# Optimization experiments

Measured on AMD Instinct MI355X. Metric: run time of the kernel, lower is better.

The kernel has to match this reference:

```python
import jax, jax.numpy as jnp
import numpy as np

B, T, C = 4, 2048, 1024
H, DK, DV = 16, 64, 64


def setup_inputs() -> dict:
    key = jax.random.key(0)
    ks = jax.random.split(key, 12)
    s = 1.0 / np.sqrt(C)
    inp = {
        "Q": jax.random.normal(ks[0], (B, T, C), jnp.float32),
        "K": jax.random.normal(ks[1], (B, T, C), jnp.float32),
        "V": jax.random.normal(ks[2], (B, T, C), jnp.float32),
        # causal mask: True (==1) means masked out
        "mask": jnp.broadcast_to(jnp.triu(jnp.ones((T, T), bool), k=1), (B, 1, T, T)),
        "Wq": jax.random.uniform(ks[3], (C, H * DK), jnp.float32, -s, s),
        "bq": jax.random.uniform(ks[4], (H * DK,), jnp.float32, -s, s),
        "Wk": jax.random.uniform(ks[5], (C, H * DK), jnp.float32, -s, s),
        "bk": jax.random.uniform(ks[6], (H * DK,), jnp.float32, -s, s),
        "Wv": jax.random.uniform(ks[7], (C, H * DV), jnp.float32, -s, s),
        "bv": jax.random.uniform(ks[8], (H * DV,), jnp.float32, -s, s),
        "Wo": jax.random.uniform(ks[9], (H * DV, C), jnp.float32, -s, s),
        "bo": jax.random.uniform(ks[10], (C,), jnp.float32, -s, s),
    }
    return inp


def _split(x, d):
    b, t, _ = x.shape
    return x.reshape(b, t, H, d).transpose(0, 2, 1, 3)  # (B,H,T,d)


def reference(Q, K, V, mask, Wq, bq, Wk, bk, Wv, bv, Wo, bo):
    Qh = _split(Q @ Wq + bq, DK)
    Kh = _split(K @ Wk + bk, DK)
    Vh = _split(V @ Wv + bv, DV)
    scores = jnp.einsum('bhqd,bhkd->bhqk', Qh, Kh) / jnp.sqrt(jnp.float32(DK))
    scores = jnp.where(mask, -jnp.inf, scores)
    attn = jax.nn.softmax(scores, axis=-1)
    out = jnp.einsum('bhqk,bhkd->bhqd', attn, Vh)
    out = out.transpose(0, 2, 1, 3).reshape(B, T, H * DV)
    return out @ Wo + bo
```

## Files before the change

kernel.cpp:

```cpp
#include <hip/hip_runtime.h>
#include <stdint.h>

#define BATCH 4
#define SEQ   2048
#define CH    1024
#define NH    16
#define HD    64

#define QSCALE 0.18033688011112042f

#define GM 8192
#define GN 1024
#define GK 1024

typedef __attribute__((ext_vector_type(8))) short bf16x8;
typedef __attribute__((ext_vector_type(4))) short bf16x4;
typedef __attribute__((ext_vector_type(4))) float f32x4;

__device__ inline unsigned short f2bf(float f) {
    unsigned u = __float_as_uint(f);
    u += 0x7fff + ((u >> 16) & 1);
    return (unsigned short)(u >> 16);
}

__device__ inline float fast_exp2(float x) {
    float r;
    asm("v_exp_f32 %0, %1" : "=v"(r) : "v"(x));
    return r;
}

__device__ inline unsigned cvt_pk_bf16(float lo, float hi) {
    unsigned r;
    asm("v_cvt_pk_bf16_f32 %0, %1, %2" : "=v"(r) : "v"(lo), "v"(hi));
    return r;
}

#if __has_builtin(__builtin_amdgcn_mfma_f32_16x16x16bf16_1k)
__device__ inline void mfma16(f32x4& c, bf16x4 a, bf16x4 b) {
    c = __builtin_amdgcn_mfma_f32_16x16x16bf16_1k(a, b, c, 0, 0, 0);
}
#else
__device__ inline void mfma16(f32x4& c, bf16x4 a, bf16x4 b) {
    asm volatile("s_nop 2\n\tv_mfma_f32_16x16x16_bf16 %0, %1, %2, %0"
                 : "+v"(c) : "v"(a), "v"(b));
}
#endif

__device__ inline void gld_lds16(const void* g, void* l) {
    __builtin_amdgcn_global_load_lds((const __attribute__((address_space(1))) void*)g,
                                     (__attribute__((address_space(3))) void*)l,
                                     16, 0, 0);
}

__global__ __launch_bounds__(256) void prep_k(
    const float* __restrict__ Wq, const float* __restrict__ Wk,
    const float* __restrict__ Wv, const float* __restrict__ Wo,
    unsigned short* __restrict__ WqT, unsigned short* __restrict__ WkT,
    unsigned short* __restrict__ WvT, unsigned short* __restrict__ WoT)
{
    __shared__ float tile[32][33];
    const int j     = blockIdx.x >> 10;
    const int local = blockIdx.x & 1023;
    const float* W = (j == 0) ? Wq : (j == 1) ? Wk : (j == 2) ? Wv : Wo;
    unsigned short* Wt = (j == 0) ? WqT : (j == 1) ? WkT : (j == 2) ? WvT : WoT;
    const int bx = (local & 31) * 32;
    const int by = (local >> 5) * 32;
    const int tx = threadIdx.x & 31;
    const int ty = threadIdx.x >> 5;
#pragma unroll
    for (int i = 0; i < 32; i += 8)
        tile[ty + i][tx] = W[(size_t)(by + ty + i) * CH + bx + tx];
    __syncthreads();
#pragma unroll
    for (int i = 0; i < 32; i += 8)
        Wt[(size_t)(bx + ty + i) * CH + by + tx] = f2bf(tile[tx][ty + i]);
}

__global__ __launch_bounds__(256, 4)
void qkv_gemm(const float* __restrict__ Qf, const float* __restrict__ Kf,
              const float* __restrict__ Vf,
              const unsigned short* __restrict__ WqT, const unsigned short* __restrict__ WkT,
              const unsigned short* __restrict__ WvT,
              const float* __restrict__ bq, const float* __restrict__ bk,
              const float* __restrict__ bv,
              unsigned short* __restrict__ Qhb, unsigned short* __restrict__ Khb,
              unsigned short* __restrict__ Vtb)
{
    __shared__ float          As32[128 * 32];
    __shared__ unsigned short Bs[128 * 32];
    const int job = blockIdx.y;
    const float* A32          = (job == 0) ? Qf  : (job == 1) ? Kf  : Vf;
    const unsigned short* Bt  = (job == 0) ? WqT : (job == 1) ? WkT : WvT;
    const float* bias         = (job == 0) ? bq  : (job == 1) ? bk  : bv;
    unsigned short* outp      = (job == 0) ? Qhb : (job == 1) ? Khb : Vtb;
    const float oscale        = (job == 0) ? QSCALE : 1.0f;

    const int tid  = threadIdx.x;
    const int lane = tid & 63;
    const int w    = tid >> 6;
    const int nbn  = GN >> 7;
    const int nbm  = GM >> 7;
    const int xcd  = blockIdx.x & 7;
    const int idx  = blockIdx.x >> 3;
    const int mb   = xcd * (nbm >> 3) + idx / nbn;
    const int nb   = idx % nbn;
    const int m0   = mb << 7;
    const int n0   = nb << 7;
    const int wrow = (w >> 1) << 6;
    const int wcol = (w & 1) << 6;
    const int lr   = lane & 15;
    const int lg   = lane >> 4;

    f32x4 acc[4][4] = {};

    for (int k0 = 0; k0 < GK; k0 += 32) {
#pragma unroll
        for (int i = 0; i < 4; ++i) {
            int chunk = i * 256 + tid;
            int row = chunk >> 3;
            int l   = (chunk & 7) ^ (row & 7);
            gld_lds16(A32 + (size_t)(m0 + row) * GK + k0 + l * 4,
                      (char*)As32 + chunk * 16);
        }
#pragma unroll
        for (int i = 0; i < 2; ++i) {
            int chunk = i * 256 + tid;
            int row = chunk >> 2;
            int l   = (chunk & 3) ^ (row & 3);
            gld_lds16(Bt + (size_t)(n0 + row) * GK + k0 + l * 8,
                      (char*)Bs + chunk * 16);
        }
        __syncthreads();

        bf16x8 af[4], bfr[4];
#pragma unroll
        for (int f = 0; f < 4; ++f) {
            const int arow = wrow + f * 16 + lr;
            const int plo  = ((lg << 1) ^ (arow & 7));
            const int phi  = plo ^ 1;
            const float* base = As32 + arow * 32;
            f32x4 lo = *(const f32x4*)(base + plo * 4);
            f32x4 hi = *(const f32x4*)(base + phi * 4);
            union { bf16x8 v; unsigned u[4]; } cv;
            cv.u[0] = cvt_pk_bf16(lo[0], lo[1]);
            cv.u[1] = cvt_pk_bf16(lo[2], lo[3]);
            cv.u[2] = cvt_pk_bf16(hi[0], hi[1]);
            cv.u[3] = cvt_pk_bf16(hi[2], hi[3]);
            af[f] = cv.v;
        }
#pragma unroll
        for (int f = 0; f < 4; ++f) {
            const int brow = wcol + f * 16 + lr;
            bfr[f] = *(const bf16x8*)(Bs + brow * 32 + ((lg ^ (brow & 3)) << 3));
        }
#pragma unroll
        for (int i = 0; i < 4; ++i)
#pragma unroll
            for (int j = 0; j < 4; ++j)
                acc[i][j] = __builtin_amdgcn_mfma_f32_16x16x32_bf16(af[i], bfr[j], acc[i][j], 0, 0, 0);
        __syncthreads();
    }

    float bvals[4];
#pragma unroll
    for (int j = 0; j < 4; ++j) bvals[j] = bias[n0 + wcol + j * 16 + lr];

    if (job < 2) {
#pragma unroll
        for (int i = 0; i < 4; ++i) {
            const int mbase = m0 + wrow + i * 16 + lg * 4;
#pragma unroll
            for (int j = 0; j < 4; ++j) {
                const int n = n0 + wcol + j * 16 + lr;
                const int h = n >> 6, d = n & 63;
#pragma unroll
                for (int r = 0; r < 4; ++r) {
                    const int m = mbase + r;
                    const int b = m >> 11, t = m & 2047;
                    outp[((size_t)(b * NH + h) * SEQ + t) * HD + d] = f2bf((acc[i][j][r] + bvals[j]) * oscale);
                }
            }
        }
    } else {
#pragma unroll
        for (int i = 0; i < 4; ++i) {
            const int mbase = m0 + wrow + i * 16 + lg * 4;
#pragma unroll
            for (int j = 0; j < 4; ++j) {
                const int n = n0 + wcol + j * 16 + lr;
                const int h = n >> 6, d = n & 63;
                const int b = mbase >> 11, t = mbase & 2047;
                union { unsigned short s[4]; uint2 v; } pk;
#pragma unroll
                for (int r = 0; r < 4; ++r) pk.s[r] = f2bf(acc[i][j][r] + bvals[j]);
                *(uint2*)(outp + ((size_t)(b * NH + h) * HD + d) * SEQ + t) = pk.v;
            }
        }
    }
}

__global__ __launch_bounds__(256, 2)
void gemm_out(const unsigned short* __restrict__ A,
              const unsigned short* __restrict__ Bt,
              const float* __restrict__ bias,
              float* __restrict__ out)
{
    __shared__ unsigned short As[128 * 64];
    __shared__ unsigned short Bs[128 * 64];
    const int tid  = threadIdx.x;
    const int lane = tid & 63;
    const int w    = tid >> 6;
    const int nbn  = GN >> 7;
    const int nbm  = GM >> 7;
    const int xcd  = blockIdx.x & 7;
    const int idx  = blockIdx.x >> 3;
    const int mb   = xcd * (nbm >> 3) + idx / nbn;
    const int nb   = idx % nbn;
    const int m0   = mb << 7;
    const int n0   = nb << 7;
    const int wrow = (w >> 1) << 6;
    const int wcol = (w & 1) << 6;
    const int lr   = lane & 15;
    const int lg   = lane >> 4;

    f32x4 acc[4][4] = {};

    for (int k0 = 0; k0 < GK; k0 += 64) {
#pragma unroll
        for (int i = 0; i < 4; ++i) {
            int chunk = i * 256 + tid;
            int row = chunk >> 3;
            int c8  = (chunk & 7) << 3;
            gld_lds16(A  + (size_t)(m0 + row) * GK + k0 + c8, (char*)As + chunk * 16);
            gld_lds16(Bt + (size_t)(n0 + row) * GK + k0 + c8, (char*)Bs + chunk * 16);
        }
        __syncthreads();
#pragma unroll
        for (int kk = 0; kk < 2; ++kk) {
            bf16x8 af[4], bfr[4];
#pragma unroll
            for (int f = 0; f < 4; ++f)
                af[f] = *(const bf16x8*)(As + (wrow + f * 16 + lr) * 64 + kk * 32 + lg * 8);
#pragma unroll
            for (int f = 0; f < 4; ++f)
                bfr[f] = *(const bf16x8*)(Bs + (wcol + f * 16 + lr) * 64 + kk * 32 + lg * 8);
#pragma unroll
            for (int i = 0; i < 4; ++i)
#pragma unroll
                for (int j = 0; j < 4; ++j)
                    acc[i][j] = __builtin_amdgcn_mfma_f32_16x16x32_bf16(af[i], bfr[j], acc[i][j], 0, 0, 0);
        }
        __syncthreads();
    }

    float bvals[4];
#pragma unroll
    for (int j = 0; j < 4; ++j) bvals[j] = bias[n0 + wcol + j * 16 + lr];

#pragma unroll
    for (int i = 0; i < 4; ++i) {
        const int mbase = m0 + wrow + i * 16 + lg * 4;
#pragma unroll
        for (int j = 0; j < 4; ++j) {
            const int n = n0 + wcol + j * 16 + lr;
#pragma unroll
            for (int r = 0; r < 4; ++r)
                out[(size_t)(mbase + r) * GN + n] = acc[i][j][r] + bvals[j];
        }
    }
}

__global__ __launch_bounds__(256, 4)
void attn_k(const unsigned short* __restrict__ Qh,
            const unsigned short* __restrict__ Kh,
            const unsigned short* __restrict__ Vt,
            unsigned short* __restrict__ O) {
    __shared__ unsigned short Ks[2][64 * 64];
    __shared__ unsigned short Vs[2][64 * 64];
    const int bh    = blockIdx.x;
    const int qtile = 31 - blockIdx.y;
    const int q0    = qtile << 6;
    const int tid  = threadIdx.x;
    const int lane = tid & 63;
    const int w    = tid >> 6;
    const int lr   = lane & 15;
    const int lg   = lane >> 4;
    const int qw   = q0 + w * 16;

    bf16x4 ones4;
#pragma unroll
    for (int j = 0; j < 4; ++j) ones4[j] = (short)0x3F80;

    bf16x8 qf[2];
#pragma unroll
    for (int kk = 0; kk < 2; ++kk)
        qf[kk] = *(const bf16x8*)(Qh + ((size_t)bh * SEQ + qw + lr) * HD + kk * 32 + lg * 8);

    float mrun = -3e38f;
    f32x4 ot[4] = {};
    f32x4 osum = {};

    const int nkt = qtile + 1;

#define STAGE(KT, B) do {                                                          \
        const int kv_ = (KT) << 6;                                                 \
        _Pragma("unroll")                                                          \
        for (int i_ = 0; i_ < 2; ++i_) {                                           \
            int c_ = i_ * 256 + tid;                                               \
            int row_ = c_ >> 3;                                                    \
            int sk_ = (((c_ & 7) ^ (row_ & 7)) << 3);                              \
            int sv_ = (((c_ & 7) ^ ((row_ >> 1) & 7)) << 3);                       \
            gld_lds16(Kh + ((size_t)bh * SEQ + kv_ + row_) * HD + sk_,             \
                      (char*)Ks[B] + c_ * 16);                                     \
            gld_lds16(Vt + ((size_t)bh * HD + row_) * SEQ + kv_ + sv_,             \
                      (char*)Vs[B] + c_ * 16);                                     \
        }                                                                          \
    } while (0)

    STAGE(0, 0);
    __syncthreads();

    for (int kt = 0; kt < nkt; ++kt) {
        if (kt + 1 < nkt) STAGE(kt + 1, (kt + 1) & 1);
        const unsigned short* Kc = Ks[kt & 1];
        const unsigned short* Vc = Vs[kt & 1];
        const int kv0 = kt << 6;

        f32x4 s[4] = {};
#pragma unroll
        for (int kk = 0; kk < 2; ++kk) {
            const int u = (((kk << 2) | lg) ^ (lr & 7)) << 3;
#pragma unroll
            for (int f = 0; f < 4; ++f) {
                bf16x8 kb = *(const bf16x8*)(Kc + (f * 16 + lr) * 64 + u);
                s[f] = __builtin_amdgcn_mfma_f32_16x16x32_bf16(kb, qf[kk], s[f], 0, 0, 0);
            }
        }

        float rmax = -3e38f;
        if (kv0 + 63 <= qw) {
#pragma unroll
            for (int f = 0; f < 4; ++f)
#pragma unroll
                for (int r = 0; r < 4; ++r) rmax = fmaxf(rmax, s[f][r]);
        } else {
            const int q = qw + lr;
#pragma unroll
            for (int f = 0; f < 4; ++f)
#pragma unroll
                for (int r = 0; r < 4; ++r) {
                    const int kv = kv0 + f * 16 + lg * 4 + r;
                    float v = (kv > q) ? -3e38f : s[f][r];
                    s[f][r] = v;
                    rmax = fmaxf(rmax, v);
                }
        }
        rmax = fmaxf(rmax, __shfl_xor(rmax, 16));
        rmax = fmaxf(rmax, __shfl_xor(rmax, 32));

        if (__any(rmax > mrun)) {
            float mn = fmaxf(mrun, rmax);
            float c  = fast_exp2(mrun - mn);
            mrun = mn;
            osum *= c;
#pragma unroll
            for (int dd = 0; dd < 4; ++dd) ot[dd] *= c;
        }

#pragma unroll
        for (int f = 0; f < 4; ++f) {
#pragma unroll
            for (int r = 0; r < 4; ++r)
                s[f][r] = fast_exp2(s[f][r] - mrun);
            union { bf16x4 v; unsigned u[2]; } pb;
            pb.u[0] = cvt_pk_bf16(s[f][0], s[f][1]);
            pb.u[1] = cvt_pk_bf16(s[f][2], s[f][3]);
            mfma16(osum, ones4, pb.v);
#pragma unroll
            for (int dd = 0; dd < 4; ++dd) {
                const int vcol = ((((f << 1) | (lg >> 1)) ^ (lr >> 1)) << 3) | ((lg & 1) << 2);
                bf16x4 va = *(const bf16x4*)(Vc + (dd * 16 + lr) * 64 + vcol);
                mfma16(ot[dd], va, pb.v);
            }
        }
        __syncthreads();
    }
#undef STAGE

    const int b = bh >> 4, h = bh & 15;
    const float inv = 1.0f / osum[0];
    const int t = qw + lr;
#pragma unroll
    for (int dd = 0; dd < 4; ++dd) {
        union { unsigned short s4[4]; uint2 v; } pk;
#pragma unroll
        for (int r = 0; r < 4; ++r) pk.s4[r] = f2bf(ot[dd][r] * inv);
        *(uint2*)(O + ((size_t)b * SEQ + t) * CH + h * HD + dd * 16 + lg * 4) = pk.v;
    }
}

extern "C" void kernel_launch(void* const* d_in, const int* in_sizes, int n_in,
                              void* d_out, int out_size, void* d_ws, size_t ws_size,
                              hipStream_t stream) {
    const float* Q  = (const float*)d_in[0];
    const float* K  = (const float*)d_in[1];
    const float* V  = (const float*)d_in[2];
    const float* Wq = (const float*)d_in[4];
    const float* bq = (const float*)d_in[5];
    const float* Wk = (const float*)d_in[6];
    const float* bk = (const float*)d_in[7];
    const float* Wv = (const float*)d_in[8];
    const float* bv = (const float*)d_in[9];
    const float* Wo = (const float*)d_in[10];
    const float* bo = (const float*)d_in[11];
    float* out = (float*)d_out;

    const size_t SZ_ACT = (size_t)BATCH * SEQ * CH;
    const size_t SZ_W   = (size_t)CH * CH;

    char* p = (char*)d_ws;
    unsigned short* WqT = (unsigned short*)p; p += SZ_W * 2;
    unsigned short* WkT = (unsigned short*)p; p += SZ_W * 2;
    unsigned short* WvT = (unsigned short*)p; p += SZ_W * 2;
    unsigned short* WoT = (unsigned short*)p; p += SZ_W * 2;
    unsigned short* Qhb = (unsigned short*)p; p += SZ_ACT * 2;
    unsigned short* Khb = (unsigned short*)p; p += SZ_ACT * 2;
    unsigned short* Vtb = (unsigned short*)p; p += SZ_ACT * 2;
    unsigned short* Ob  = (unsigned short*)p; p += SZ_ACT * 2;

    prep_k<<<4096, 256, 0, stream>>>(Wq, Wk, Wv, Wo, WqT, WkT, WvT, WoT);

    qkv_gemm<<<dim3((GM / 128) * (GN / 128), 3), 256, 0, stream>>>(
        Q, K, V, WqT, WkT, WvT, bq, bk, bv, Qhb, Khb, Vtb);

    attn_k<<<dim3(BATCH * NH, SEQ / 64), 256, 0, stream>>>(Qhb, Khb, Vtb, Ob);

    gemm_out<<<(GM / 128) * (GN / 128), 256, 0, stream>>>(Ob, WoT, bo, out);
}
```

Before: 185.0 us.

## Double-buffer QKV GEMM LDS tiles and lazily rescale softmax max

The QKV projection GEMM now keeps two LDS buffers and issues the global-to-LDS loads for the next K tile before computing the current one, so load latency can overlap the MFMA work. This doubles the kernel's shared memory, and the launch-bounds occupancy hint drops from 4 to 2 blocks to match. Separately, the flash-attention loop only rescales its running max and accumulators when a new row max exceeds the stored max by more than 8 in log2 units, skipping most rescale branches. That relies on bf16/fp32 headroom for exp2 values up to 256, which adds some risk of precision loss or overflow.

```diff
diff --git a/kernel.cpp b/kernel.cpp
--- a/kernel.cpp
+++ b/kernel.cpp
@@ -76,7 +76,7 @@
         Wt[(size_t)(bx + ty + i) * CH + by + tx] = f2bf(tile[tx][ty + i]);
 }
 
-__global__ __launch_bounds__(256, 4)
+__global__ __launch_bounds__(256, 2)
 void qkv_gemm(const float* __restrict__ Qf, const float* __restrict__ Kf,
               const float* __restrict__ Vf,
               const unsigned short* __restrict__ WqT, const unsigned short* __restrict__ WkT,
@@ -86,8 +86,8 @@
               unsigned short* __restrict__ Qhb, unsigned short* __restrict__ Khb,
               unsigned short* __restrict__ Vtb)
 {
-    __shared__ float          As32[128 * 32];
-    __shared__ unsigned short Bs[128 * 32];
+    __shared__ float          As32[2][128 * 32];
+    __shared__ unsigned short Bs[2][128 * 32];
     const int job = blockIdx.y;
     const float* A32          = (job == 0) ? Qf  : (job == 1) ? Kf  : Vf;
     const unsigned short* Bt  = (job == 0) ? WqT : (job == 1) ? WkT : WvT;
@@ -113,24 +113,33 @@
 
     f32x4 acc[4][4] = {};
 
-    for (int k0 = 0; k0 < GK; k0 += 32) {
-#pragma unroll
-        for (int i = 0; i < 4; ++i) {
-            int chunk = i * 256 + tid;
-            int row = chunk >> 3;
-            int l   = (chunk & 7) ^ (row & 7);
-            gld_lds16(A32 + (size_t)(m0 + row) * GK + k0 + l * 4,
-                      (char*)As32 + chunk * 16);
-        }
-#pragma unroll
-        for (int i = 0; i < 2; ++i) {
-            int chunk = i * 256 + tid;
-            int row = chunk >> 2;
-            int l   = (chunk & 3) ^ (row & 3);
-            gld_lds16(Bt + (size_t)(n0 + row) * GK + k0 + l * 8,
-                      (char*)Bs + chunk * 16);
-        }
-        __syncthreads();
+#define QSTAGE(K0, B) do {                                                         \
+        _Pragma("unroll")                                                          \
+        for (int i_ = 0; i_ < 4; ++i_) {                                           \
+            int c_ = i_ * 256 + tid;                                               \
+            int row_ = c_ >> 3;                                                    \
+            int l_   = (c_ & 7) ^ (row_ & 7);                                      \
+            gld_lds16(A32 + (size_t)(m0 + row_) * GK + (K0) + l_ * 4,              \
+                      (char*)As32[B] + c_ * 16);                                   \
+        }                                                                          \
+        _Pragma("unroll")                                                          \
+        for (int i_ = 0; i_ < 2; ++i_) {                                           \
+            int c_ = i_ * 256 + tid;                                               \
+            int row_ = c_ >> 2;                                                    \
+            int l_   = (c_ & 3) ^ (row_ & 3);                                      \
+            gld_lds16(Bt + (size_t)(n0 + row_) * GK + (K0) + l_ * 8,               \
+                      (char*)Bs[B] + c_ * 16);                                     \
+        }                                                                          \
+    } while (0)
+
+    QSTAGE(0, 0);
+    __syncthreads();
+
+    const int nkt = GK / 32;
+    for (int kt = 0; kt < nkt; ++kt) {
+        if (kt + 1 < nkt) QSTAGE((kt + 1) * 32, (kt + 1) & 1);
+        const float*          Ac = As32[kt & 1];
+        const unsigned short* Bc = Bs[kt & 1];
 
         bf16x8 af[4], bfr[4];
 #pragma unroll
@@ -138,7 +147,7 @@
             const int arow = wrow + f * 16 + lr;
             const int plo  = ((lg << 1) ^ (arow & 7));
             const int phi  = plo ^ 1;
-            const float* base = As32 + arow * 32;
+            const float* base = Ac + arow * 32;
             f32x4 lo = *(const f32x4*)(base + plo * 4);
             f32x4 hi = *(const f32x4*)(base + phi * 4);
             union { bf16x8 v; unsigned u[4]; } cv;
@@ -151,7 +160,7 @@
 #pragma unroll
         for (int f = 0; f < 4; ++f) {
             const int brow = wcol + f * 16 + lr;
-            bfr[f] = *(const bf16x8*)(Bs + brow * 32 + ((lg ^ (brow & 3)) << 3));
+            bfr[f] = *(const bf16x8*)(Bc + brow * 32 + ((lg ^ (brow & 3)) << 3));
         }
 #pragma unroll
         for (int i = 0; i < 4; ++i)
@@ -160,6 +169,7 @@
                 acc[i][j] = __builtin_amdgcn_mfma_f32_16x16x32_bf16(af[i], bfr[j], acc[i][j], 0, 0, 0);
         __syncthreads();
     }
+#undef QSTAGE
 
     float bvals[4];
 #pragma unroll
@@ -358,7 +368,7 @@
         rmax = fmaxf(rmax, __shfl_xor(rmax, 16));
         rmax = fmaxf(rmax, __shfl_xor(rmax, 32));
 
-        if (__any(rmax > mrun)) {
+        if (!__all(rmax <= mrun + 8.0f)) {
             float mn = fmaxf(mrun, rmax);
             float c  = fast_exp2(mrun - mn);
             mrun = mn;
```

Result: no change. 182.7 us (-1.2%).
